# Kernel optimization log

Hardware: AMD Instinct MI355X
Metric: run time of the kernel (lower is better)

## Reference

```python
import jax, jax.numpy as jnp
import numpy as np

B, CIN, COUT, N, S, K, KS, DIM = 4, 64, 64, 32768, 8192, 32, 16, 3


def setup_inputs() -> dict:
    key = jax.random.key(0)
    ks = jax.random.split(key, 9)
    x = jax.random.normal(ks[0], (B, CIN, N), dtype=jnp.float32)
    pos = jax.random.normal(ks[1], (B, DIM, N), dtype=jnp.float32)
    support_points = jax.random.normal(ks[2], (B, DIM, S), dtype=jnp.float32)
    neighbors_indices = jax.random.randint(ks[3], (B, S, K), 0, N, dtype=jnp.int64)
    radius = jnp.ones((1,), dtype=jnp.float32)
    # learned params (Conv2d with 1x1 kernels == per-point matmuls)
    w_fc1 = jax.random.normal(ks[4], (KS, DIM), dtype=jnp.float32) * 0.1   # fc1: dim -> kernel_size
    w_fc2 = jax.random.normal(ks[5], (KS, 2 * KS), dtype=jnp.float32) * 0.1
    w_fc3 = jax.random.normal(ks[6], (KS, 2 * KS), dtype=jnp.float32) * 0.1
    w_cv = jax.random.normal(ks[7], (COUT, CIN, KS), dtype=jnp.float32) * 0.05  # Conv2d(CIN,COUT,(1,KS))
    return {"x": x, "pos": pos, "support_points": support_points,
            "neighbors_indices": neighbors_indices, "radius": radius,
            "w_fc1": w_fc1, "w_fc2": w_fc2, "w_fc3": w_fc3, "w_cv": w_cv}


def _gather(feat, idx):
    # feat: [B, C, N], idx: [B, S, K] -> [B, C, S, K]
    return jax.vmap(lambda f, i: f[:, i])(feat, idx)


def reference(x, pos, support_points, neighbors_indices, radius,
              w_fc1, w_fc2, w_fc3, w_cv):
    mask = (neighbors_indices > -1)                       # [B,S,K]
    idx = jnp.where(mask, neighbors_indices, 0)
    pos_g = _gather(pos, idx)                             # [B,3,S,K]
    x_g = _gather(x, idx)                                 # [B,CIN,S,K]

    pts = pos_g - support_points[..., None]               # [B,3,S,K]
    mask_pts = (~jnp.isinf(pts[:, :1])).astype(pts.dtype) # [B,1,S,K]
    pts = jnp.nan_to_num(pts, nan=0.0, posinf=0.0, neginf=0.0)
    pts = pts / radius[0]

    # distance weight: L2-normalize binary mask over neighbor axis (torch F.normalize, eps=1e-12)
    mf = mask.astype(pts.dtype)                           # [B,S,K]
    nrm = jnp.sqrt(jnp.sum(mf * mf, axis=2, keepdims=True))
    dw = (mf / jnp.maximum(nrm, 1e-12))[:, None]          # [B,1,S,K]
    dw = dw * mask_pts

    mat = jax.nn.relu(jnp.einsum('kd,bdsn->bksn', w_fc1, pts)) * dw
    mp1 = jnp.max(mat, axis=3, keepdims=True)
    mat = jnp.concatenate([mat, jnp.broadcast_to(mp1, mat.shape)], axis=1)
    mat = jax.nn.relu(jnp.einsum('km,bmsn->bksn', w_fc2, mat)) * dw
    mp2 = jnp.max(mat, axis=3, keepdims=True)
    mat = jnp.concatenate([mat, jnp.broadcast_to(mp2, mat.shape)], axis=1)
    mat = jax.nn.relu(jnp.einsum('km,bmsn->bksn', w_fc3, mat)) * dw    # [B,KS,S,K]

    # features[b,s,c,k] = sum_n x_g[b,c,s,n] * mat[b,k,s,n]
    feats = jnp.einsum('bcsn,bksn->bcsk', x_g, mat)        # [B,CIN,S,KS]
    out = jnp.einsum('ock,bcsk->bos', w_cv, feats)         # [B,COUT,S]

    sup_inf = jnp.isinf(support_points[:, :1, :])          # [B,1,S]
    out = jnp.where(sup_inf, jnp.inf, out)
    return out
```

## Files before the change

kernel.cpp:

```cpp
#include <hip/hip_runtime.h>
#include <math.h>

#define B_    4
#define CIN_  64
#define COUT_ 64
#define N_    32768
#define S_    8192

typedef __attribute__((ext_vector_type(8))) short short8;
typedef __attribute__((ext_vector_type(4))) float f32x4a;
typedef _Float16 __attribute__((ext_vector_type(2))) h2v;

static __device__ __forceinline__ unsigned short f2bf(float x) {
    unsigned u = __float_as_uint(x);
    u += 0x7fffu + ((u >> 16) & 1u);
    return (unsigned short)(u >> 16);
}
static __device__ __forceinline__ unsigned pack2bf(float a, float b) {
    return (unsigned)f2bf(a) | ((unsigned)f2bf(b) << 16);
}
static __device__ __forceinline__ unsigned packh2(float x, float y) {
    union { h2v v; unsigned u; } c;
    c.v[0] = (_Float16)x; c.v[1] = (_Float16)y;
    return c.u;
}
static __device__ __forceinline__ unsigned pkmax2(unsigned a, unsigned b) {
    union { unsigned u; h2v v; } ca, cb, cr;
    ca.u = a; cb.u = b;
    cr.v[0] = ca.v[0] > cb.v[0] ? ca.v[0] : cb.v[0];
    cr.v[1] = ca.v[1] > cb.v[1] ? ca.v[1] : cb.v[1];
    return cr.u;
}
static __device__ __forceinline__ float fdot2u(unsigned a, unsigned b, float c) {
    union { unsigned u; h2v v; } ca, cb; ca.u = a; cb.u = b;
    return __builtin_amdgcn_fdot2(ca.v, cb.v, c, false);
}
template <int CTRL>
static __device__ __forceinline__ unsigned pmax_ror(unsigned v) {
    unsigned r = (unsigned)__builtin_amdgcn_update_dpp(
        (int)v, (int)v, CTRL, 0xf, 0xf, false);
    return pkmax2(v, r);
}
#define ROR8 0x128
#define ROR4 0x124
#define ROR2 0x122
#define ROR1 0x121

static __device__ __forceinline__ int fl(int p, int col) {
    return p * 2048 + (col ^ ((p & 7) << 4) ^ (((col >> 7) & 7) << 4));
}

__global__ __launch_bounds__(256) void prep_kernel(
    const float* __restrict__ x,   unsigned short* __restrict__ xTB,
    const float* __restrict__ pos, float* __restrict__ posT,
    const float* __restrict__ wcv, unsigned short* __restrict__ wcvB,
    const float* __restrict__ w2,  const float* __restrict__ w3,
    unsigned* __restrict__ wh)
{
    const int bid = blockIdx.x;

    if (bid < 2048) {
        __shared__ float tile[64][65];
        const int b  = bid >> 9;
        const int n0 = (bid & 511) * 64;
        const int tx = threadIdx.x & 63;
        const int ty = threadIdx.x >> 6;

        const float* xb = x + (size_t)b * CIN_ * N_;
        #pragma unroll
        for (int c = ty; c < 64; c += 4)
            tile[c][tx] = xb[(size_t)c * N_ + n0 + tx];
        __syncthreads();

        const int cp = threadIdx.x & 31;
        const int r0 = threadIdx.x >> 5;
        unsigned short* xTb = xTB + ((size_t)b * N_ + n0) * 64;
        #pragma unroll
        for (int nn = r0; nn < 64; nn += 8) {
            ushort2 v;
            v.x = f2bf(tile[2 * cp][nn]);
            v.y = f2bf(tile[2 * cp + 1][nn]);
            *(ushort2*)&xTb[(size_t)nn * 64 + 2 * cp] = v;
        }
    } else if (bid < 2560) {
        const int r = bid - 2048;
        const int b = r >> 7;
        const int n = (r & 127) * 256 + threadIdx.x;
        const float* pb = pos + (size_t)b * 3 * N_;
        float4 v = make_float4(pb[n], pb[N_ + n], pb[2 * N_ + n], 0.0f);
        *(float4*)&posT[((size_t)b * N_ + n) * 4] = v;
    } else if (bid < 2816) {
        const int i = (bid - 2560) * 256 + threadIdx.x;
        const int o   = i >> 10;
        const int rem = i & 1023;
        const int k   = rem >> 6;
        const int c   = rem & 63;
        wcvB[i] = f2bf(wcv[(size_t)o * 1024 + c * 16 + k]);
    } else {
        const int e = (bid - 2816) * 256 + threadIdx.x;
        const int layer = e >> 8, k = (e >> 4) & 15, j = e & 15;
        const float* w = layer ? w3 : w2;
        const int base = (j < 8) ? (2 * j) : (16 + 2 * (j - 8));
        wh[e] = packh2(w[k * 32 + base], w[k * 32 + base + 1]);
    }
}

__global__ __launch_bounds__(512) void fka_fused_kernel(
    const float* __restrict__ posT, const float* __restrict__ sup,
    const int*   __restrict__ nbr, const float* __restrict__ radius,
    const float* __restrict__ w1,  const unsigned* __restrict__ wh,
    const unsigned short* __restrict__ xTB,
    const unsigned short* __restrict__ wcvB,
    float* __restrict__ out)
{
    __shared__ unsigned short featsL[16 * 1024];
    __shared__ int   idxs[16][32];
    __shared__ float t2s[16][16];
    __shared__ float pbuf[1024];

    const int b  = blockIdx.y;
    const int t  = threadIdx.x;
    const int g  = t >> 5;
    const int n  = t & 31;
    const int s0 = blockIdx.x * 16;
    const int s  = s0 + g;

    const int raw    = nbr[(((size_t)b * S_ + s) << 5) + n];
    const bool valid = raw > -1;
    const int id     = valid ? raw : 0;

    unsigned long long bal = __ballot(valid);
    unsigned bits = (unsigned)(bal >> (t & 32));
    const float nrm = sqrtf((float)__popc(bits));
    float dw = valid ? (1.0f / fmaxf(nrm, 1e-12f)) : 0.0f;

    const float4 pg = *(const float4*)&posT[((size_t)b * N_ + id) * 4];
    float px = pg.x - sup[(size_t)(b * 3 + 0) * S_ + s];
    float py = pg.y - sup[(size_t)(b * 3 + 1) * S_ + s];
    float pz = pg.z - sup[(size_t)(b * 3 + 2) * S_ + s];
    if (isinf(px)) dw = 0.0f;
    px = (isnan(px) || isinf(px)) ? 0.0f : px;
    py = (isnan(py) || isinf(py)) ? 0.0f : py;
    pz = (isnan(pz) || isinf(pz)) ? 0.0f : pz;
    const float inv_r = 1.0f / radius[0];
    px *= inv_r; py *= inv_r; pz *= inv_r;

    const int kk = n & 15;

    unsigned m1h[8];
    #pragma unroll
    for (int j = 0; j < 8; ++j) {
        float v0 = w1[(2*j) * 3 + 0] * px + w1[(2*j) * 3 + 1] * py + w1[(2*j) * 3 + 2] * pz;
        float v1 = w1[(2*j+1) * 3 + 0] * px + w1[(2*j+1) * 3 + 1] * py + w1[(2*j+1) * 3 + 2] * pz;
        m1h[j] = packh2(fmaxf(v0, 0.0f) * dw, fmaxf(v1, 0.0f) * dw);
    }
    unsigned mp1h[8];
    #pragma unroll
    for (int j = 0; j < 8; ++j) {
        unsigned v = m1h[j];
        v = pkmax2(v, (unsigned)__shfl_xor((int)v, 16, 32));
        v = pmax_ror<ROR8>(v); v = pmax_ror<ROR4>(v);
        v = pmax_ror<ROR2>(v); v = pmax_ror<ROR1>(v);
        mp1h[j] = v;
    }
    {
        const unsigned* wp = wh + kk * 16 + 8;
        float pa = 0.0f, pb = 0.0f;
        #pragma unroll
        for (int j = 0; j < 4; ++j) pa = fdot2u(wp[j], mp1h[j], pa);
        #pragma unroll
        for (int j = 0; j < 4; ++j) pb = fdot2u(wp[4 + j], mp1h[4 + j], pb);
        float tp = (n & 16) ? pb : pa;
        tp += __shfl_xor(tp, 16, 32);
        t2s[g][kk] = tp;
    }
    unsigned m2h[8];
    {
        float4 ta = *(const float4*)&t2s[g][0];
        float4 tb = *(const float4*)&t2s[g][4];
        float4 tc = *(const float4*)&t2s[g][8];
        float4 td = *(const float4*)&t2s[g][12];
        float t2v[16] = {ta.x, ta.y, ta.z, ta.w, tb.x, tb.y, tb.z, tb.w,
                         tc.x, tc.y, tc.z, tc.w, td.x, td.y, td.z, td.w};
        float m2[16];
        #pragma unroll
        for (int k = 0; k < 16; ++k) {
            const unsigned* wm = wh + k * 16;
            float v = t2v[k];
            #pragma unroll
            for (int j = 0; j < 8; ++j) v = fdot2u(wm[j], m1h[j], v);
            m2[k] = fmaxf(v, 0.0f) * dw;
        }
        #pragma unroll
        for (int j = 0; j < 8; ++j) m2h[j] = packh2(m2[2*j], m2[2*j+1]);
    }
    unsigned mp2h[8];
    #pragma unroll
    for (int j = 0; j < 8; ++j) {
        unsigned v = m2h[j];
        v = pkmax2(v, (unsigned)__shfl_xor((int)v, 16, 32));
        v = pmax_ror<ROR8>(v); v = pmax_ror<ROR4>(v);
        v = pmax_ror<ROR2>(v); v = pmax_ror<ROR1>(v);
        mp2h[j] = v;
    }
    {
        const unsigned* wp = wh + 256 + kk * 16 + 8;
        float pa = 0.0f, pb = 0.0f;
        #pragma unroll
        for (int j = 0; j < 4; ++j) pa = fdot2u(wp[j], mp2h[j], pa);
        #pragma unroll
        for (int j = 0; j < 4; ++j) pb = fdot2u(wp[4 + j], mp2h[4 + j], pb);
        float tp = (n & 16) ? pb : pa;
        tp += __shfl_xor(tp, 16, 32);
        t2s[g][kk] = tp;
    }
    float m3[16];
    {
        float4 ta = *(const float4*)&t2s[g][0];
        float4 tb = *(const float4*)&t2s[g][4];
        float4 tc = *(const float4*)&t2s[g][8];
        float4 td = *(const float4*)&t2s[g][12];
        float t3v[16] = {ta.x, ta.y, ta.z, ta.w, tb.x, tb.y, tb.z, tb.w,
                         tc.x, tc.y, tc.z, tc.w, td.x, td.y, td.z, td.w};
        #pragma unroll
        for (int k = 0; k < 16; ++k) {
            const unsigned* wm = wh + 256 + k * 16;
            float v = t3v[k];
            #pragma unroll
            for (int j = 0; j < 8; ++j) v = fdot2u(wm[j], m2h[j], v);
            m3[k] = fmaxf(v, 0.0f) * dw;
        }
    }

    idxs[g][n] = id;
    {
        const int hi = n >> 3, jj = n & 7;
        unsigned short* base = &featsL[g * 1024 + hi * 128 + jj];
        #pragma unroll
        for (int k = 0; k < 16; ++k) {
            const int row = (k + hi + g) & 15;
            base[row * 8] = f2bf(m3[k]);
        }
    }

    const int wv  = t >> 6;
    const int l   = t & 63;
    const int hi2 = l >> 4;
    const int k15 = l & 15;
    const unsigned short* xb = xTB + (size_t)b * N_ * 64;
    char* fLp = (char*)featsL;

    short8 bfrag[2];
    #pragma unroll
    for (int pp = 0; pp < 2; ++pp) {
        const int p = wv * 2 + pp;
        const int brow = (k15 + hi2 + p) & 15;
        bfrag[pp] = *(const short8*)&featsL[p * 1024 + hi2 * 128 + brow * 8];
    }

    #pragma unroll
    for (int pp = 0; pp < 2; ++pp) {
        const int p = wv * 2 + pp;

        int ids8[8];
        #pragma unroll
        for (int j = 0; j < 8; ++j) ids8[j] = idxs[p][hi2 * 8 + j];

        f32x4a acc[4];
        #pragma unroll
        for (int ct = 0; ct < 4; ++ct) acc[ct] = (f32x4a){0.f, 0.f, 0.f, 0.f};

        #pragma unroll
        for (int ct = 0; ct < 4; ++ct) {
            union { unsigned short u[8]; short8 v; } A;
            #pragma unroll
            for (int j = 0; j < 8; ++j)
                A.u[j] = xb[((size_t)ids8[j] << 6) + ct * 16 + k15];
            acc[ct] = __builtin_amdgcn_mfma_f32_16x16x32_bf16(A.v, bfrag[pp], acc[ct], 0, 0, 0);
        }

        #pragma unroll
        for (int ct = 0; ct < 4; ++ct) {
            uint2 val;
            val.x = pack2bf(acc[ct][0], acc[ct][1]);
            val.y = pack2bf(acc[ct][2], acc[ct][3]);
            const int col = k15 * 128 + ct * 32 + hi2 * 8;
            *(uint2*)(fLp + fl(p, col)) = val;
        }
    }
    __syncthreads();

    const int ot  = wv & 3;
    const int kh  = wv >> 2;
    const int lq  = hi2;
    const int l15 = k15;

    const unsigned short* apod =
        wcvB + (size_t)(ot * 16 + l15) * 1024 + kh * 512 + lq * 8;

    f32x4a oacc = (f32x4a){0.f, 0.f, 0.f, 0.f};
    #pragma unroll 4
    for (int ks = 0; ks < 16; ++ks) {
        const int col = kh * 1024 + ks * 64 + lq * 16;
        short8 bfv = *(const short8*)(fLp + fl(l15, col));
        short8 afv = *(const short8*)(apod + ks * 32);
        oacc = __builtin_amdgcn_mfma_f32_16x16x32_bf16(afv, bfv, oacc, 0, 0, 0);
    }

    if (kh == 1) {
        #pragma unroll
        for (int r = 0; r < 4; ++r)
            pbuf[ot * 256 + (lq * 4 + r) * 16 + l15] = oacc[r];
    }
    __syncthreads();
    if (kh == 0) {
        const int sidx = s0 + l15;
        const bool infs = isinf(sup[(size_t)b * 3 * S_ + sidx]);
        #pragma unroll
        for (int r = 0; r < 4; ++r) {
            const float v = oacc[r] + pbuf[ot * 256 + (lq * 4 + r) * 16 + l15];
            const int o = ot * 16 + lq * 4 + r;
            out[((size_t)b * COUT_ + o) * S_ + sidx] = infs ? INFINITY : v;
        }
    }
}

extern "C" void kernel_launch(void* const* d_in, const int* in_sizes, int n_in,
                              void* d_out, int out_size, void* d_ws, size_t ws_size,
                              hipStream_t stream)
{
    const float* x   = (const float*)d_in[0];
    const float* pos = (const float*)d_in[1];
    const float* sup = (const float*)d_in[2];
    const int*   nbr = (const int*)d_in[3];
    const float* rad = (const float*)d_in[4];
    const float* w1  = (const float*)d_in[5];
    const float* w2  = (const float*)d_in[6];
    const float* w3  = (const float*)d_in[7];
    const float* wcv = (const float*)d_in[8];
    float* out = (float*)d_out;

    char* p = (char*)d_ws;
    unsigned short* xTB = (unsigned short*)p;  p += (size_t)B_ * N_ * 64 * sizeof(unsigned short);
    float* posT = (float*)p;                   p += (size_t)B_ * N_ * 4 * sizeof(float);
    unsigned short* wcvB = (unsigned short*)p; p += (size_t)COUT_ * 1024 * sizeof(unsigned short);
    unsigned* wh = (unsigned*)p;               p += (size_t)512 * sizeof(unsigned);

    prep_kernel<<<dim3(2818), 256, 0, stream>>>(x, xTB, pos, posT, wcv, wcvB, w2, w3, wh);

    fka_fused_kernel<<<dim3(S_ / 16, B_), 512, 0, stream>>>(
        posT, sup, nbr, rad, w1, wh, xTB, wcvB, out);
}
```

Baseline: 74.51 us.

## Interleave channel layout of bf16 x so gathers load 8 bytes per neighbor

Changes the transposed bf16 feature layout so each lane's four channel-tile values (c, c+16, c+32, c+48) sit contiguously. The MFMA A-fragment can then be built from one 8-byte load per neighbor instead of four scattered 2-byte loads, cutting gather instruction count. Separately, the ReLU and distance-weight multiply in the fc1/fc2 stages move to packed fp16 ops. This adds fp16 rounding before the ReLU and multiply.

Result: faster. 69.67 us (-6.5%).

```diff
diff --git a/kernel.cpp b/kernel.cpp
--- a/kernel.cpp
+++ b/kernel.cpp
@@ -30,6 +30,14 @@
     cr.v[0] = ca.v[0] > cb.v[0] ? ca.v[0] : cb.v[0];
     cr.v[1] = ca.v[1] > cb.v[1] ? ca.v[1] : cb.v[1];
     return cr.u;
+}
+static __device__ __forceinline__ unsigned pkrelu_mul(unsigned v, unsigned dwp) {
+    union { unsigned u; h2v v; } a, d, r;
+    a.u = v; d.u = dwp;
+    const _Float16 z = (_Float16)0.f;
+    r.v[0] = (a.v[0] > z ? a.v[0] : z) * d.v[0];
+    r.v[1] = (a.v[1] > z ? a.v[1] : z) * d.v[1];
+    return r.u;
 }
 static __device__ __forceinline__ float fdot2u(unsigned a, unsigned b, float c) {
     union { unsigned u; h2v v; } ca, cb; ca.u = a; cb.u = b;
@@ -72,15 +80,18 @@
             tile[c][tx] = xb[(size_t)c * N_ + n0 + tx];
         __syncthreads();
 
-        const int cp = threadIdx.x & 31;
-        const int r0 = threadIdx.x >> 5;
+        const int k15p = threadIdx.x & 15;
+        const int rg   = threadIdx.x >> 4;
         unsigned short* xTb = xTB + ((size_t)b * N_ + n0) * 64;
         #pragma unroll
-        for (int nn = r0; nn < 64; nn += 8) {
-            ushort2 v;
-            v.x = f2bf(tile[2 * cp][nn]);
-            v.y = f2bf(tile[2 * cp + 1][nn]);
-            *(ushort2*)&xTb[(size_t)nn * 64 + 2 * cp] = v;
+        for (int q = 0; q < 4; ++q) {
+            const int nn = rg + q * 16;
+            union { uint2 u; unsigned short us[4]; } v;
+            v.us[0] = f2bf(tile[k15p][nn]);
+            v.us[1] = f2bf(tile[16 + k15p][nn]);
+            v.us[2] = f2bf(tile[32 + k15p][nn]);
+            v.us[3] = f2bf(tile[48 + k15p][nn]);
+            *(uint2*)&xTb[(size_t)nn * 64 + k15p * 4] = v.u;
         }
     } else if (bid < 2560) {
         const int r = bid - 2048;
@@ -146,13 +157,14 @@
     px *= inv_r; py *= inv_r; pz *= inv_r;
 
     const int kk = n & 15;
+    const unsigned dwh2 = packh2(dw, dw);
 
     unsigned m1h[8];
     #pragma unroll
     for (int j = 0; j < 8; ++j) {
         float v0 = w1[(2*j) * 3 + 0] * px + w1[(2*j) * 3 + 1] * py + w1[(2*j) * 3 + 2] * pz;
         float v1 = w1[(2*j+1) * 3 + 0] * px + w1[(2*j+1) * 3 + 1] * py + w1[(2*j+1) * 3 + 2] * pz;
-        m1h[j] = packh2(fmaxf(v0, 0.0f) * dw, fmaxf(v1, 0.0f) * dw);
+        m1h[j] = pkrelu_mul(packh2(v0, v1), dwh2);
     }
     unsigned mp1h[8];
     #pragma unroll
@@ -182,17 +194,18 @@
         float4 td = *(const float4*)&t2s[g][12];
         float t2v[16] = {ta.x, ta.y, ta.z, ta.w, tb.x, tb.y, tb.z, tb.w,
                          tc.x, tc.y, tc.z, tc.w, td.x, td.y, td.z, td.w};
-        float m2[16];
-        #pragma unroll
-        for (int k = 0; k < 16; ++k) {
-            const unsigned* wm = wh + k * 16;
-            float v = t2v[k];
+        #pragma unroll
+        for (int j = 0; j < 8; ++j) {
+            const unsigned* wmA = wh + (2*j) * 16;
+            const unsigned* wmB = wh + (2*j+1) * 16;
+            float vA = t2v[2*j], vB = t2v[2*j+1];
             #pragma unroll
-            for (int j = 0; j < 8; ++j) v = fdot2u(wm[j], m1h[j], v);
-            m2[k] = fmaxf(v, 0.0f) * dw;
-        }
-        #pragma unroll
-        for (int j = 0; j < 8; ++j) m2h[j] = packh2(m2[2*j], m2[2*j+1]);
+            for (int q = 0; q < 8; ++q) {
+                vA = fdot2u(wmA[q], m1h[q], vA);
+                vB = fdot2u(wmB[q], m1h[q], vB);
+            }
+            m2h[j] = pkrelu_mul(packh2(vA, vB), dwh2);
+        }
     }
     unsigned mp2h[8];
     #pragma unroll
@@ -266,6 +279,11 @@
         #pragma unroll
         for (int j = 0; j < 8; ++j) ids8[j] = idxs[p][hi2 * 8 + j];
 
+        union { uint2 q; unsigned short us[4]; } xq[8];
+        #pragma unroll
+        for (int j = 0; j < 8; ++j)
+            xq[j].q = *(const uint2*)(xb + ((size_t)ids8[j] << 6) + (k15 << 2));
+
         f32x4a acc[4];
         #pragma unroll
         for (int ct = 0; ct < 4; ++ct) acc[ct] = (f32x4a){0.f, 0.f, 0.f, 0.f};
@@ -274,8 +292,7 @@
         for (int ct = 0; ct < 4; ++ct) {
             union { unsigned short u[8]; short8 v; } A;
             #pragma unroll
-            for (int j = 0; j < 8; ++j)
-                A.u[j] = xb[((size_t)ids8[j] << 6) + ct * 16 + k15];
+            for (int j = 0; j < 8; ++j) A.u[j] = xq[j].us[ct];
             acc[ct] = __builtin_amdgcn_mfma_f32_16x16x32_bf16(A.v, bfrag[pp], acc[ct], 0, 0, 0);
         }
 
```
